# Performance work log

Measured on AMD Instinct MI355X. Metric: run time of the kernel, lower is better.

The kernel has to match this reference:

```python
import jax, jax.numpy as jnp
from jax import lax
import numpy as np

TWO_PI = 2.0 * np.pi

# ---- batched real-amplitude statevector simulator (RY/CNOT only -> real state) ----

def _init_state(batch, n):
    s = jnp.zeros((batch, 2 ** n), dtype=jnp.float32).at[:, 0].set(1.0)
    return s.reshape((batch,) + (2,) * n)

def _ry(state, wire, theta, n):
    # state: (B, 2,...,2); theta: scalar or (B,)
    ax = wire + 1
    h = theta * 0.5
    c = jnp.reshape(jnp.cos(h), (-1,) + (1,) * (n - 1))
    s = jnp.reshape(jnp.sin(h), (-1,) + (1,) * (n - 1))
    s0 = lax.index_in_dim(state, 0, ax, keepdims=False)
    s1 = lax.index_in_dim(state, 1, ax, keepdims=False)
    return jnp.stack([c * s0 - s * s1, s * s0 + c * s1], axis=ax)

def _cnot(state, ctrl, tgt):
    axc, axt = ctrl + 1, tgt + 1
    s0 = lax.index_in_dim(state, 0, axc, keepdims=True)
    s1 = lax.index_in_dim(state, 1, axc, keepdims=True)
    return jnp.concatenate([s0, jnp.flip(s1, axis=axt)], axis=axc)

def _expz(state, wire, n):
    sgn = jnp.reshape(jnp.array([1.0, -1.0], state.dtype),
                      (1,) * (wire + 1) + (2,) + (1,) * (n - wire - 1))
    return jnp.sum(state * state * sgn, axis=tuple(range(1, n + 1)))

# gate lists: ('ry', theta_index, wire) or ('cx', control, target)
EDGE_OPS = [('ry',0,0),('ry',1,1),('cx',0,1),('ry',2,2),('ry',3,3),('cx',3,2),
            ('ry',4,4),('ry',5,5),('cx',4,5),('ry',6,6),('ry',7,7),('cx',7,6),
            ('ry',8,1),('ry',9,2),('cx',1,2),('ry',10,5),('ry',11,6),('cx',6,5),
            ('ry',12,2),('ry',13,5),('cx',2,5),('ry',14,5)]

NODE_OPS = [('ry',0,0),('ry',1,1),('cx',0,1),('ry',2,2),('ry',3,3),('cx',3,2),
            ('ry',4,4),('ry',5,5),('cx',4,5),('ry',6,6),('ry',7,7),('cx',7,6),
            ('ry',8,8),('ry',9,9),('cx',8,9),('ry',10,10),('ry',11,11),('cx',11,10),
            ('ry',12,1),('ry',13,2),('cx',1,2),('ry',14,5),('ry',15,6),('cx',6,5),
            ('ry',16,9),('ry',17,10),('cx',10,9),('ry',18,2),('ry',19,5),('cx',2,5),
            ('ry',20,5),('ry',21,9),('cx',5,9),('ry',22,4)]

def _circuit(angles, theta, ops, n, meas_wire):
    st = _init_state(angles.shape[0], n)
    for i in range(n):  # input encoding RYs, per-sample angles
        st = _ry(st, i, angles[:, i], n)
    for op in ops:
        if op[0] == 'ry':
            st = _ry(st, op[2], theta[op[1]], n)
        else:
            st = _cnot(st, op[1], op[2])
    return _expz(st, meas_wire, n)

# ---- GNN pieces ----

def _edge_net(H, Ri, Ro, theta):
    bo = Ro.T @ H                      # [E,4]
    bi = Ri.T @ H                      # [E,4]
    B = jnp.concatenate([bo, bi], axis=1)  # [E,8]
    return (1.0 - _circuit(B, theta, EDGE_OPS, 8, 5)) * 0.5

def _node_net(H, e, Ri, Ro, theta):
    bo = Ro.T @ H                      # [E,4]
    bi = Ri.T @ H                      # [E,4]
    mi = (Ri * e[None, :]) @ bo        # [N,4]
    mo = (Ro * e[None, :]) @ bi        # [N,4]
    M = jnp.concatenate([mi, mo, H], axis=1)  # [N,12]
    return jnp.pi * (1.0 - _circuit(M, theta, NODE_OPS, 12, 9))

def _gnn(X, Ri, Ro, W_in, b_in, theta_edge, theta_node, n_iters=2):
    H = jnp.concatenate([jax.nn.sigmoid(X @ W_in + b_in) * TWO_PI, X], axis=1)  # [N,4]
    e = _edge_net(H, Ri, Ro, theta_edge)
    for _ in range(n_iters):
        h = _node_net(H, e, Ri, Ro, theta_node)   # [N]
        H = jnp.concatenate([h[:, None], X], axis=1)
        e = _edge_net(H, Ri, Ro, theta_edge)
    return e


def setup_inputs() -> dict:
    key = jax.random.key(0)
    ks = jax.random.split(key, 6)
    N, E = 2048, 4096
    X = jax.random.normal(ks[0], (N, 3), jnp.float32)
    recv = jax.random.randint(ks[1], (E,), 0, N)
    send = jax.random.randint(ks[2], (E,), 0, N)
    cols = jnp.arange(E)
    Ri = jnp.zeros((N, E), jnp.float32).at[recv, cols].set(1.0)
    Ro = jnp.zeros((N, E), jnp.float32).at[send, cols].set(1.0)
    W_in = jax.random.normal(ks[3], (3, 1), jnp.float32)
    b_in = jnp.zeros((1,), jnp.float32)
    theta_edge = jax.random.uniform(ks[4], (15,), jnp.float32, 0.0, TWO_PI)
    theta_node = jax.random.uniform(ks[5], (23,), jnp.float32, 0.0, TWO_PI)
    return {'X': X, 'Ri': Ri, 'Ro': Ro, 'W_in': W_in, 'b_in': b_in,
            'theta_edge': theta_edge, 'theta_node': theta_node}


def reference(X, Ri, Ro, W_in, b_in, theta_edge, theta_node):
    return _gnn(X, Ri, Ro, W_in, b_in, theta_edge, theta_node, n_iters=2)
```

## Files before the change

kernel.cpp:

```cpp
#include <hip/hip_runtime.h>
#include <math.h>

#define N_NODES 2048
#define N_EDGES 4096
#define PI_F 3.14159265358979323846f
#define TWO_PI_F 6.28318530717958647692f

#define EDGE_BLKS 16
#define NODE_BLKS 8
#define TOTAL_BLKS 256
#define SCAN_BLKS (TOTAL_BLKS - EDGE_BLKS)
#define SCAN_STRIDE (SCAN_BLKS * 256)
#define TOT4 (N_NODES * N_EDGES / 4)

__device__ __forceinline__ float agent_load(const float* p) {
    return __hip_atomic_load(p, __ATOMIC_RELAXED, __HIP_MEMORY_SCOPE_AGENT);
}
__device__ __forceinline__ int agent_load_i(const int* p) {
    return __hip_atomic_load(p, __ATOMIC_RELAXED, __HIP_MEMORY_SCOPE_AGENT);
}
__device__ __forceinline__ void agent_store(float* p, float v) {
    __hip_atomic_store(p, v, __ATOMIC_RELAXED, __HIP_MEMORY_SCOPE_AGENT);
}
__device__ __forceinline__ void agent_store_i(int* p, int v) {
    __hip_atomic_store(p, v, __ATOMIC_RELAXED, __HIP_MEMORY_SCOPE_AGENT);
}
__device__ __forceinline__ void spin_ge(const int* p, int v) {
    while (__hip_atomic_load(p, __ATOMIC_RELAXED, __HIP_MEMORY_SCOPE_AGENT) < v)
        __builtin_amdgcn_s_sleep(2);
    asm volatile("" ::: "memory");
}
__device__ __forceinline__ int spin_idx(const int* p) {
    int v;
    while ((v = agent_load_i(p)) == 0) __builtin_amdgcn_s_sleep(2);
    asm volatile("" ::: "memory");
    return v - 1;
}


template<int M>
__device__ __forceinline__ void ry16(float* a, float c, float s) {
#pragma unroll
    for (int i = 0; i < 16; ++i)
        if (!(i & M)) {
            int j = i | M;
            float x0 = a[i], x1 = a[j];
            a[i] = c * x0 - s * x1;
            a[j] = s * x0 + c * x1;
        }
}
template<int MC, int MT>
__device__ __forceinline__ void cx16(float* a) {
#pragma unroll
    for (int i = 0; i < 16; ++i)
        if ((i & MC) && !(i & MT)) {
            int j = i | MT;
            float t = a[i]; a[i] = a[j]; a[j] = t;
        }
}

template<bool BTYPE>
__device__ __forceinline__ void sub16(const float* ic, const float* is,
                                      const float* thc, const float* ths,
                                      float& z, float& x) {
    float a[16];
    a[0] = ic[3]; a[1] = is[3];
#pragma unroll
    for (int i = 0; i < 2; ++i) { a[i | 2] = a[i] * is[2]; a[i] *= ic[2]; }
#pragma unroll
    for (int i = 0; i < 4; ++i) { a[i | 4] = a[i] * is[1]; a[i] *= ic[1]; }
#pragma unroll
    for (int i = 0; i < 8; ++i) { a[i | 8] = a[i] * is[0]; a[i] *= ic[0]; }
    ry16<8>(a, thc[0], ths[0]);
    ry16<4>(a, thc[1], ths[1]);
    cx16<8, 4>(a);
    ry16<2>(a, thc[2], ths[2]);
    ry16<1>(a, thc[3], ths[3]);
    cx16<1, 2>(a);
    ry16<4>(a, thc[4], ths[4]);
    ry16<2>(a, thc[5], ths[5]);
    if (BTYPE) { cx16<2, 4>(a); ry16<4>(a, thc[6], ths[6]); }
    else       { cx16<4, 2>(a); ry16<2>(a, thc[6], ths[6]); }
    const int m = BTYPE ? 4 : 2;
    z = 0.f; x = 0.f;
#pragma unroll
    for (int i = 0; i < 16; ++i) z += (i & m) ? -a[i] * a[i] : a[i] * a[i];
    if (BTYPE) {
#pragma unroll
        for (int i = 0; i < 16; ++i) if (!(i & 4)) x += a[i] * a[i | 4];
        x *= 2.f;
    }
}

__device__ __forceinline__ void edge_pub(
        float chh, float shh, const float* cxv, const float* sxv,
        const float* teC, const float* teS,
        float& zA, float& zB, float& xB) {
    float ic[4] = {chh, cxv[0], cxv[1], cxv[2]};
    float is[4] = {shh, sxv[0], sxv[1], sxv[2]};
    float dmy;
    {
        float thc[7] = {teC[0], teC[1], teC[2], teC[3], teC[8], teC[9], teC[12]};
        float ths[7] = {teS[0], teS[1], teS[2], teS[3], teS[8], teS[9], teS[12]};
        sub16<false>(ic, is, thc, ths, zA, dmy);
    }
    {
        float thc[7] = {teC[4], teC[5], teC[6], teC[7], teC[10], teC[11], teC[13]};
        float ths[7] = {teS[4], teS[5], teS[6], teS[7], teS[10], teS[11], teS[13]};
        sub16<true>(ic, is, thc, ths, zB, xB);
    }
}

__device__ __forceinline__ void scatter8(float ev, const float4& Hs, const float4& Hr,
                                         int si, int ri,
                                         float* __restrict__ macc, int* __restrict__ arr) {
    atomicAdd(&macc[ri*8+0], ev*Hs.x); atomicAdd(&macc[ri*8+1], ev*Hs.y);
    atomicAdd(&macc[ri*8+2], ev*Hs.z); atomicAdd(&macc[ri*8+3], ev*Hs.w);
    atomicAdd(&macc[si*8+4], ev*Hr.x); atomicAdd(&macc[si*8+5], ev*Hr.y);
    atomicAdd(&macc[si*8+6], ev*Hr.z); atomicAdd(&macc[si*8+7], ev*Hr.w);
    asm volatile("s_waitcnt vmcnt(0)" ::: "memory");
    atomicAdd(&arr[ri], 1); atomicAdd(&arr[si], 1);
}

__global__ __launch_bounds__(256, 1) void k_fused(
        const float* __restrict__ X, const float* __restrict__ Ri,
        const float* __restrict__ Ro, const float* __restrict__ W,
        const float* __restrict__ b, const float* __restrict__ te,
        const float* __restrict__ tn,
        float* __restrict__ H, float* __restrict__ pub,
        int* __restrict__ send, int* __restrict__ recv,
        float* __restrict__ maccA, float* __restrict__ maccB,
        int* __restrict__ arrA, int* __restrict__ arrB,
        int* __restrict__ epoch, int* __restrict__ inited,
        int* __restrict__ deg, int* __restrict__ sdone,
        float* __restrict__ out) {
    int blk = blockIdx.x, tid = threadIdx.x;

    if (blk < EDGE_BLKS) {
        int e = blk * 256 + tid;
        float c14h, s14h;
        __sincosf(0.5f * te[14], &s14h, &c14h);
        float C14 = c14h*c14h - s14h*s14h;
        float S14 = 2.f*c14h*s14h;

        int si = spin_idx(send + e);
        int ri = spin_idx(recv + e);
        spin_ge(inited + si, 1);
        spin_ge(inited + ri, 1);
        float4 Hs, Hr;
        Hs.x = agent_load(H+si*4+0); Hs.y = agent_load(H+si*4+1);
        Hs.z = agent_load(H+si*4+2); Hs.w = agent_load(H+si*4+3);
        Hr.x = agent_load(H+ri*4+0); Hr.y = agent_load(H+ri*4+1);
        Hr.z = agent_load(H+ri*4+2); Hr.w = agent_load(H+ri*4+3);

        float zA = agent_load(&pub[si*4+0]);
        float zB = agent_load(&pub[ri*4+1]);
        float xB = agent_load(&pub[ri*4+2]);
        float ev = 0.5f*(1.f - (C14*zA*zB - S14*xB));
        scatter8(ev, Hs, Hr, si, ri, maccA, arrA);

        spin_ge(epoch + si, 1); spin_ge(epoch + ri, 1);
        zA = agent_load(&pub[si*4+0]);
        zB = agent_load(&pub[ri*4+1]);
        xB = agent_load(&pub[ri*4+2]);
        Hs.x = agent_load(&H[si*4]);
        Hr.x = agent_load(&H[ri*4]);
        ev = 0.5f*(1.f - (C14*zA*zB - S14*xB));
        scatter8(ev, Hs, Hr, si, ri, maccB, arrB);

        spin_ge(epoch + si, 2); spin_ge(epoch + ri, 2);
        zA = agent_load(&pub[si*4+0]);
        zB = agent_load(&pub[ri*4+1]);
        xB = agent_load(&pub[ri*4+2]);
        out[e] = 0.5f*(1.f - (C14*zA*zB - S14*xB));
        return;
    }

    bool is_node = (blk < EDGE_BLKS + NODE_BLKS);
    int n = (blk - EDGE_BLKS) * 256 + tid;
    float chh, shh, cxv[3], sxv[3];
    float teC[14], teS[14], tnC[22], tnS[22];
    if (is_node) {
        float x0 = X[n*3+0], x1 = X[n*3+1], x2 = X[n*3+2];
        float z = x0*W[0] + x1*W[1] + x2*W[2] + b[0];
        float sg = 1.0f / (1.0f + __expf(-z));
        float h = sg * TWO_PI_F;
        __sincosf(0.5f*h,  &shh, &chh);
        __sincosf(0.5f*x0, &sxv[0], &cxv[0]);
        __sincosf(0.5f*x1, &sxv[1], &cxv[1]);
        __sincosf(0.5f*x2, &sxv[2], &cxv[2]);
#pragma unroll
        for (int k = 0; k < 14; ++k) __sincosf(0.5f*te[k], &teS[k], &teC[k]);
#pragma unroll
        for (int k = 0; k < 22; ++k) __sincosf(0.5f*tn[k], &tnS[k], &tnC[k]);
        float zA, zB, xB;
        edge_pub(chh, shh, cxv, sxv, teC, teS, zA, zB, xB);
        agent_store(&pub[n*4+0], zA);
        agent_store(&pub[n*4+1], zB);
        agent_store(&pub[n*4+2], xB);
        agent_store(&H[n*4+0], h);
        agent_store(&H[n*4+1], x0);
        agent_store(&H[n*4+2], x2 == x2 ? x1 : x1);
        agent_store(&H[n*4+3], x2);
        asm volatile("s_waitcnt vmcnt(0)" ::: "memory");
        agent_store_i(inited + n, 1);
    }

    {
        int gid = (blk - EDGE_BLKS) * 256 + tid;
        const float4* Ri4 = (const float4*)Ri;
        const float4* Ro4 = (const float4*)Ro;
        for (int t0 = gid; t0 < TOT4; t0 += 4 * SCAN_STRIDE) {
            float4 vi[4], vo[4];
#pragma unroll
            for (int u = 0; u < 4; ++u) {
                int t = t0 + u * SCAN_STRIDE;
                if (t < TOT4) { vi[u] = Ri4[t]; vo[u] = Ro4[t]; }
            }
#pragma unroll
            for (int u = 0; u < 4; ++u) {
                int t = t0 + u * SCAN_STRIDE;
                if (t < TOT4) {
                    int base = t * 4;
                    int row = base >> 12;
                    int e   = base & (N_EDGES - 1);
                    int cnt = 0;
                    if (vi[u].x != 0.f) { agent_store_i(recv+e+0, row+1); ++cnt; }
                    if (vi[u].y != 0.f) { agent_store_i(recv+e+1, row+1); ++cnt; }
                    if (vi[u].z != 0.f) { agent_store_i(recv+e+2, row+1); ++cnt; }
                    if (vi[u].w != 0.f) { agent_store_i(recv+e+3, row+1); ++cnt; }
                    if (vo[u].x != 0.f) { agent_store_i(send+e+0, row+1); ++cnt; }
                    if (vo[u].y != 0.f) { agent_store_i(send+e+1, row+1); ++cnt; }
                    if (vo[u].z != 0.f) { agent_store_i(send+e+2, row+1); ++cnt; }
                    if (vo[u].w != 0.f) { agent_store_i(send+e+3, row+1); ++cnt; }
                    if (cnt) atomicAdd(&deg[row], cnt);
                }
            }
        }
        asm volatile("s_waitcnt vmcnt(0)" ::: "memory");
        __syncthreads();
        if (tid == 0) atomicAdd(sdone, 1);
    }
    if (!is_node) return;

    spin_ge(sdone, SCAN_BLKS);
    int dg = agent_load_i(deg + n);
    float C20 = tnC[20]*tnC[20] - tnS[20]*tnS[20];
    float S20 = 2.f*tnC[20]*tnS[20];

    for (int it = 0; it < 2; ++it) {
        const float* mc_ = it ? maccB : maccA;
        const int*   ar  = it ? arrB  : arrA;
        spin_ge(ar + n, dg);
        float M[8], mC[8], mS[8];
#pragma unroll
        for (int k = 0; k < 8; ++k) M[k] = agent_load(mc_ + n*8 + k);
#pragma unroll
        for (int k = 0; k < 8; ++k) __sincosf(0.5f*M[k], &mS[k], &mC[k]);
        float zA1, zA2, xA2, zB9, dmy;
        {
            float thc[7] = {tnC[0],tnC[1],tnC[2],tnC[3],tnC[12],tnC[13],tnC[18]};
            float ths[7] = {tnS[0],tnS[1],tnS[2],tnS[3],tnS[12],tnS[13],tnS[18]};
            sub16<false>(&mC[0], &mS[0], thc, ths, zA1, dmy);
        }
        {
            float thc[7] = {tnC[4],tnC[5],tnC[6],tnC[7],tnC[14],tnC[15],tnC[19]};
            float ths[7] = {tnS[4],tnS[5],tnS[6],tnS[7],tnS[14],tnS[15],tnS[19]};
            sub16<true>(&mC[4], &mS[4], thc, ths, zA2, xA2);
        }
        {
            float ic[4] = {chh, cxv[0], cxv[1], cxv[2]};
            float is[4] = {shh, sxv[0], sxv[1], sxv[2]};
            float thc[7] = {tnC[8],tnC[9],tnC[10],tnC[11],tnC[16],tnC[17],tnC[21]};
            float ths[7] = {tnS[8],tnS[9],tnS[10],tnS[11],tnS[16],tnS[17],tnS[21]};
            sub16<true>(ic, is, thc, ths, zB9, dmy);
        }
        float p9 = (C20*zA1*zA2 - S20*xA2) * zB9;
        float h = PI_F * (1.f - p9);
        __sincosf(0.5f*h, &shh, &chh);
        float zAe, zBe, xBe;
        edge_pub(chh, shh, cxv, sxv, teC, teS, zAe, zBe, xBe);
        agent_store(&pub[n*4+0], zAe);
        agent_store(&pub[n*4+1], zBe);
        agent_store(&pub[n*4+2], xBe);
        agent_store(&H[n*4], h);
        asm volatile("s_waitcnt vmcnt(0)" ::: "memory");
        agent_store_i(epoch + n, it + 1);
    }
}

extern "C" void kernel_launch(void* const* d_in, const int* in_sizes, int n_in,
                              void* d_out, int out_size, void* d_ws, size_t ws_size,
                              hipStream_t stream) {
    const float* X  = (const float*)d_in[0];
    const float* Ri = (const float*)d_in[1];
    const float* Ro = (const float*)d_in[2];
    const float* W  = (const float*)d_in[3];
    const float* b  = (const float*)d_in[4];
    const float* te = (const float*)d_in[5];
    const float* tn = (const float*)d_in[6];
    float* out = (float*)d_out;

    float* H     = (float*)d_ws;
    float* pub   = H + N_NODES * 4;
    int*   send  = (int*)(pub + N_NODES * 4);
    int*   recv  = send + N_EDGES;
    float* maccA = (float*)(recv + N_EDGES);
    float* maccB = maccA + N_NODES * 8;
    int*   arrA  = (int*)(maccB + N_NODES * 8);
    int*   arrB  = arrA + N_NODES;
    int*   epoch = arrB + N_NODES;
    int*   inited= epoch + N_NODES;
    int*   deg   = inited + N_NODES;
    int*   sdone = deg + N_NODES;
    size_t zbytes = (size_t)(2*N_EDGES + 4*N_NODES*8 + 5*N_NODES + 16) * 4;

    hipMemsetAsync((void*)send, 0, zbytes, stream);
    k_fused<<<TOTAL_BLKS, 256, 0, stream>>>(X, Ri, Ro, W, b, te, tn,
                                            H, pub, send, recv,
                                            maccA, maccB, arrA, arrB,
                                            epoch, inited, deg, sdone, out);
}
```

Measured before the change: 137.3 us.

## Spread adjacency scan over all blocks and use 64-lane edge/node actors

All 256 blocks now scan the dense Ri/Ro incidence matrices, where before 16 blocks were reserved as edge spinners. Edge and node work moves to single-wavefront actors spread across 64 and 32 blocks, which start after a grid-wide scan-complete barrier. The per-edge index spins and the inited flags are dropped, so send and recv no longer need zeroing and the memset shrinks. The node loop also computes the message-independent zB9 subcircuit before spinning on arrivals. In exchange, edge work cannot overlap the scan, and removing the min-blocks launch bound relies on all 256 blocks being co-resident for the spin barrier.

```diff
diff --git a/kernel.cpp b/kernel.cpp
--- a/kernel.cpp
+++ b/kernel.cpp
@@ -6,11 +6,9 @@
 #define PI_F 3.14159265358979323846f
 #define TWO_PI_F 6.28318530717958647692f
 
-#define EDGE_BLKS 16
-#define NODE_BLKS 8
-#define TOTAL_BLKS 256
-#define SCAN_BLKS (TOTAL_BLKS - EDGE_BLKS)
-#define SCAN_STRIDE (SCAN_BLKS * 256)
+#define NBLK 256
+#define NTHR 256
+#define NSCAN (NBLK * NTHR)
 #define TOT4 (N_NODES * N_EDGES / 4)
 
 __device__ __forceinline__ float agent_load(const float* p) {
@@ -29,12 +27,6 @@
     while (__hip_atomic_load(p, __ATOMIC_RELAXED, __HIP_MEMORY_SCOPE_AGENT) < v)
         __builtin_amdgcn_s_sleep(2);
     asm volatile("" ::: "memory");
-}
-__device__ __forceinline__ int spin_idx(const int* p) {
-    int v;
-    while ((v = agent_load_i(p)) == 0) __builtin_amdgcn_s_sleep(2);
-    asm volatile("" ::: "memory");
-    return v - 1;
 }
 
 
@@ -122,7 +114,7 @@
     atomicAdd(&arr[ri], 1); atomicAdd(&arr[si], 1);
 }
 
-__global__ __launch_bounds__(256, 1) void k_fused(
+__global__ __launch_bounds__(256) void k_fused(
         const float* __restrict__ X, const float* __restrict__ Ri,
         const float* __restrict__ Ro, const float* __restrict__ W,
         const float* __restrict__ b, const float* __restrict__ te,
@@ -131,22 +123,91 @@
         int* __restrict__ send, int* __restrict__ recv,
         float* __restrict__ maccA, float* __restrict__ maccB,
         int* __restrict__ arrA, int* __restrict__ arrB,
-        int* __restrict__ epoch, int* __restrict__ inited,
-        int* __restrict__ deg, int* __restrict__ sdone,
-        float* __restrict__ out) {
+        int* __restrict__ epoch, int* __restrict__ deg,
+        int* __restrict__ sdone, float* __restrict__ out) {
     int blk = blockIdx.x, tid = threadIdx.x;
-
-    if (blk < EDGE_BLKS) {
-        int e = blk * 256 + tid;
-        float c14h, s14h;
-        __sincosf(0.5f * te[14], &s14h, &c14h);
-        float C14 = c14h*c14h - s14h*s14h;
-        float S14 = 2.f*c14h*s14h;
-
-        int si = spin_idx(send + e);
-        int ri = spin_idx(recv + e);
-        spin_ge(inited + si, 1);
-        spin_ge(inited + ri, 1);
+    bool edge_actor = (blk < 64)              && (tid < 64);
+    bool node_actor = (blk >= 64 && blk < 96) && (tid < 64);
+
+    float chh = 0.f, shh = 0.f, cxv[3], sxv[3];
+    float teC[14], teS[14], tnC[22], tnS[22];
+    float C14 = 0.f, S14 = 0.f;
+
+    if (edge_actor) {
+        float c, s;
+        __sincosf(0.5f * te[14], &s, &c);
+        C14 = c*c - s*s;
+        S14 = 2.f*c*s;
+    }
+    if (node_actor) {
+        int n = (blk - 64) * 64 + tid;
+        float x0 = X[n*3+0], x1 = X[n*3+1], x2 = X[n*3+2];
+        float z = x0*W[0] + x1*W[1] + x2*W[2] + b[0];
+        float sg = 1.0f / (1.0f + __expf(-z));
+        float h = sg * TWO_PI_F;
+        __sincosf(0.5f*h,  &shh, &chh);
+        __sincosf(0.5f*x0, &sxv[0], &cxv[0]);
+        __sincosf(0.5f*x1, &sxv[1], &cxv[1]);
+        __sincosf(0.5f*x2, &sxv[2], &cxv[2]);
+#pragma unroll
+        for (int k = 0; k < 14; ++k) __sincosf(0.5f*te[k], &teS[k], &teC[k]);
+#pragma unroll
+        for (int k = 0; k < 22; ++k) __sincosf(0.5f*tn[k], &tnS[k], &tnC[k]);
+        float zA, zB, xB;
+        edge_pub(chh, shh, cxv, sxv, teC, teS, zA, zB, xB);
+        agent_store(&pub[n*4+0], zA);
+        agent_store(&pub[n*4+1], zB);
+        agent_store(&pub[n*4+2], xB);
+        agent_store(&H[n*4+0], h);
+        agent_store(&H[n*4+1], x0);
+        agent_store(&H[n*4+2], x1);
+        agent_store(&H[n*4+3], x2);
+    }
+
+    {
+        int gid = blk * NTHR + tid;
+        const float4* Ri4 = (const float4*)Ri;
+        const float4* Ro4 = (const float4*)Ro;
+#pragma unroll 1
+        for (int t0 = gid; t0 < TOT4; t0 += 4 * NSCAN) {
+            float4 vi[4], vo[4];
+#pragma unroll
+            for (int u = 0; u < 4; ++u) {
+                int t = t0 + u * NSCAN;
+                vi[u] = Ri4[t]; vo[u] = Ro4[t];
+            }
+#pragma unroll
+            for (int u = 0; u < 4; ++u) {
+                int t = t0 + u * NSCAN;
+                int base = t * 4;
+                int row = base >> 12;
+                int e   = base & (N_EDGES - 1);
+                int cnt = 0;
+                if (vi[u].x != 0.f) { agent_store_i(recv+e+0, row); ++cnt; }
+                if (vi[u].y != 0.f) { agent_store_i(recv+e+1, row); ++cnt; }
+                if (vi[u].z != 0.f) { agent_store_i(recv+e+2, row); ++cnt; }
+                if (vi[u].w != 0.f) { agent_store_i(recv+e+3, row); ++cnt; }
+                if (vo[u].x != 0.f) { agent_store_i(send+e+0, row); ++cnt; }
+                if (vo[u].y != 0.f) { agent_store_i(send+e+1, row); ++cnt; }
+                if (vo[u].z != 0.f) { agent_store_i(send+e+2, row); ++cnt; }
+                if (vo[u].w != 0.f) { agent_store_i(send+e+3, row); ++cnt; }
+                if (cnt) atomicAdd(&deg[row], cnt);
+            }
+        }
+        asm volatile("s_waitcnt vmcnt(0)" ::: "memory");
+        __syncthreads();
+        if (tid == 0) atomicAdd(sdone, 1);
+    }
+
+    if (!edge_actor && !node_actor) return;
+    int lane = tid;
+
+    spin_ge(sdone, NBLK);
+
+    if (edge_actor) {
+        int e = blk * 64 + lane;
+        int si = agent_load_i(send + e);
+        int ri = agent_load_i(recv + e);
         float4 Hs, Hr;
         Hs.x = agent_load(H+si*4+0); Hs.y = agent_load(H+si*4+1);
         Hs.z = agent_load(H+si*4+2); Hs.w = agent_load(H+si*4+3);
@@ -176,74 +237,7 @@
         return;
     }
 
-    bool is_node = (blk < EDGE_BLKS + NODE_BLKS);
-    int n = (blk - EDGE_BLKS) * 256 + tid;
-    float chh, shh, cxv[3], sxv[3];
-    float teC[14], teS[14], tnC[22], tnS[22];
-    if (is_node) {
-        float x0 = X[n*3+0], x1 = X[n*3+1], x2 = X[n*3+2];
-        float z = x0*W[0] + x1*W[1] + x2*W[2] + b[0];
-        float sg = 1.0f / (1.0f + __expf(-z));
-        float h = sg * TWO_PI_F;
-        __sincosf(0.5f*h,  &shh, &chh);
-        __sincosf(0.5f*x0, &sxv[0], &cxv[0]);
-        __sincosf(0.5f*x1, &sxv[1], &cxv[1]);
-        __sincosf(0.5f*x2, &sxv[2], &cxv[2]);
-#pragma unroll
-        for (int k = 0; k < 14; ++k) __sincosf(0.5f*te[k], &teS[k], &teC[k]);
-#pragma unroll
-        for (int k = 0; k < 22; ++k) __sincosf(0.5f*tn[k], &tnS[k], &tnC[k]);
-        float zA, zB, xB;
-        edge_pub(chh, shh, cxv, sxv, teC, teS, zA, zB, xB);
-        agent_store(&pub[n*4+0], zA);
-        agent_store(&pub[n*4+1], zB);
-        agent_store(&pub[n*4+2], xB);
-        agent_store(&H[n*4+0], h);
-        agent_store(&H[n*4+1], x0);
-        agent_store(&H[n*4+2], x2 == x2 ? x1 : x1);
-        agent_store(&H[n*4+3], x2);
-        asm volatile("s_waitcnt vmcnt(0)" ::: "memory");
-        agent_store_i(inited + n, 1);
-    }
-
-    {
-        int gid = (blk - EDGE_BLKS) * 256 + tid;
-        const float4* Ri4 = (const float4*)Ri;
-        const float4* Ro4 = (const float4*)Ro;
-        for (int t0 = gid; t0 < TOT4; t0 += 4 * SCAN_STRIDE) {
-            float4 vi[4], vo[4];
-#pragma unroll
-            for (int u = 0; u < 4; ++u) {
-                int t = t0 + u * SCAN_STRIDE;
-                if (t < TOT4) { vi[u] = Ri4[t]; vo[u] = Ro4[t]; }
-            }
-#pragma unroll
-            for (int u = 0; u < 4; ++u) {
-                int t = t0 + u * SCAN_STRIDE;
-                if (t < TOT4) {
-                    int base = t * 4;
-                    int row = base >> 12;
-                    int e   = base & (N_EDGES - 1);
-                    int cnt = 0;
-                    if (vi[u].x != 0.f) { agent_store_i(recv+e+0, row+1); ++cnt; }
-                    if (vi[u].y != 0.f) { agent_store_i(recv+e+1, row+1); ++cnt; }
-                    if (vi[u].z != 0.f) { agent_store_i(recv+e+2, row+1); ++cnt; }
-                    if (vi[u].w != 0.f) { agent_store_i(recv+e+3, row+1); ++cnt; }
-                    if (vo[u].x != 0.f) { agent_store_i(send+e+0, row+1); ++cnt; }
-                    if (vo[u].y != 0.f) { agent_store_i(send+e+1, row+1); ++cnt; }
-                    if (vo[u].z != 0.f) { agent_store_i(send+e+2, row+1); ++cnt; }
-                    if (vo[u].w != 0.f) { agent_store_i(send+e+3, row+1); ++cnt; }
-                    if (cnt) atomicAdd(&deg[row], cnt);
-                }
-            }
-        }
-        asm volatile("s_waitcnt vmcnt(0)" ::: "memory");
-        __syncthreads();
-        if (tid == 0) atomicAdd(sdone, 1);
-    }
-    if (!is_node) return;
-
-    spin_ge(sdone, SCAN_BLKS);
+    int n = (blk - 64) * 64 + lane;
     int dg = agent_load_i(deg + n);
     float C20 = tnC[20]*tnC[20] - tnS[20]*tnS[20];
     float S20 = 2.f*tnC[20]*tnS[20];
@@ -251,29 +245,30 @@
     for (int it = 0; it < 2; ++it) {
         const float* mc_ = it ? maccB : maccA;
         const int*   ar  = it ? arrB  : arrA;
-        spin_ge(ar + n, dg);
-        float M[8], mC[8], mS[8];
-#pragma unroll
-        for (int k = 0; k < 8; ++k) M[k] = agent_load(mc_ + n*8 + k);
-#pragma unroll
-        for (int k = 0; k < 8; ++k) __sincosf(0.5f*M[k], &mS[k], &mC[k]);
-        float zA1, zA2, xA2, zB9, dmy;
-        {
-            float thc[7] = {tnC[0],tnC[1],tnC[2],tnC[3],tnC[12],tnC[13],tnC[18]};
-            float ths[7] = {tnS[0],tnS[1],tnS[2],tnS[3],tnS[12],tnS[13],tnS[18]};
-            sub16<false>(&mC[0], &mS[0], thc, ths, zA1, dmy);
-        }
-        {
-            float thc[7] = {tnC[4],tnC[5],tnC[6],tnC[7],tnC[14],tnC[15],tnC[19]};
-            float ths[7] = {tnS[4],tnS[5],tnS[6],tnS[7],tnS[14],tnS[15],tnS[19]};
-            sub16<true>(&mC[4], &mS[4], thc, ths, zA2, xA2);
-        }
+        float zB9, dmy;
         {
             float ic[4] = {chh, cxv[0], cxv[1], cxv[2]};
             float is[4] = {shh, sxv[0], sxv[1], sxv[2]};
             float thc[7] = {tnC[8],tnC[9],tnC[10],tnC[11],tnC[16],tnC[17],tnC[21]};
             float ths[7] = {tnS[8],tnS[9],tnS[10],tnS[11],tnS[16],tnS[17],tnS[21]};
             sub16<true>(ic, is, thc, ths, zB9, dmy);
+        }
+        spin_ge(ar + n, dg);
+        float M[8], mC[8], mS[8];
+#pragma unroll
+        for (int k = 0; k < 8; ++k) M[k] = agent_load(mc_ + n*8 + k);
+#pragma unroll
+        for (int k = 0; k < 8; ++k) __sincosf(0.5f*M[k], &mS[k], &mC[k]);
+        float zA1, zA2, xA2;
+        {
+            float thc[7] = {tnC[0],tnC[1],tnC[2],tnC[3],tnC[12],tnC[13],tnC[18]};
+            float ths[7] = {tnS[0],tnS[1],tnS[2],tnS[3],tnS[12],tnS[13],tnS[18]};
+            sub16<false>(&mC[0], &mS[0], thc, ths, zA1, dmy);
+        }
+        {
+            float thc[7] = {tnC[4],tnC[5],tnC[6],tnC[7],tnC[14],tnC[15],tnC[19]};
+            float ths[7] = {tnS[4],tnS[5],tnS[6],tnS[7],tnS[14],tnS[15],tnS[19]};
+            sub16<true>(&mC[4], &mS[4], thc, ths, zA2, xA2);
         }
         float p9 = (C20*zA1*zA2 - S20*xA2) * zB9;
         float h = PI_F * (1.f - p9);
@@ -310,14 +305,13 @@
     int*   arrA  = (int*)(maccB + N_NODES * 8);
     int*   arrB  = arrA + N_NODES;
     int*   epoch = arrB + N_NODES;
-    int*   inited= epoch + N_NODES;
-    int*   deg   = inited + N_NODES;
+    int*   deg   = epoch + N_NODES;
     int*   sdone = deg + N_NODES;
-    size_t zbytes = (size_t)(2*N_EDGES + 4*N_NODES*8 + 5*N_NODES + 16) * 4;
-
-    hipMemsetAsync((void*)send, 0, zbytes, stream);
-    k_fused<<<TOTAL_BLKS, 256, 0, stream>>>(X, Ri, Ro, W, b, te, tn,
-                                            H, pub, send, recv,
-                                            maccA, maccB, arrA, arrB,
-                                            epoch, inited, deg, sdone, out);
-}
+    size_t zbytes = (size_t)(2*N_NODES*8 + 4*N_NODES + 16) * 4;
+
+    hipMemsetAsync((void*)maccA, 0, zbytes, stream);
+    k_fused<<<NBLK, NTHR, 0, stream>>>(X, Ri, Ro, W, b, te, tn,
+                                       H, pub, send, recv,
+                                       maccA, maccB, arrA, arrB,
+                                       epoch, deg, sdone, out);
+}
```

Measured after the change: 129.0 us. 1.06x faster.
